# Kernel tuning notes

Hardware: AMD Instinct MI355X
Metric: run time of the kernel (lower is better)

## Reference

```python
import jax, jax.numpy as jnp
import numpy as np

N = 30000      # nodes
E = 480000     # edges
NF = 92        # node features
EF = 50        # edge features
D1 = 64        # dim1
D2 = 64        # dim2
L = 3          # conv_count
FC = 2         # fc_count
G = 256        # graphs in batch
EPS = 1e-5


def setup_inputs() -> dict:
    key = jax.random.key(0)
    ks = jax.random.split(key, 20)
    s = 0.05
    zd = 2 * D1 + EF  # CGConv concat dim
    inp = {
        "x": jax.random.normal(ks[0], (N, NF), jnp.float32),
        "edge_attr": jax.random.uniform(ks[1], (E, EF), jnp.float32),
        "lin0_w": jax.random.normal(ks[2], (NF, D1), jnp.float32) * s,
        "lin0_b": jnp.zeros((D1,), jnp.float32),
        "conv_wf": jax.random.normal(ks[3], (L, zd, D1), jnp.float32) * s,
        "conv_bf": jnp.zeros((L, D1), jnp.float32),
        "conv_ws": jax.random.normal(ks[4], (L, zd, D1), jnp.float32) * s,
        "conv_bs": jnp.zeros((L, D1), jnp.float32),
        "bn_gamma": jnp.ones((L, D1), jnp.float32),
        "bn_beta": jnp.zeros((L, D1), jnp.float32),
        "lin1_w": jax.random.normal(ks[5], (D1, D2), jnp.float32) * s,
        "lin1_b": jnp.zeros((D2,), jnp.float32),
        "fc_w": jax.random.normal(ks[6], (FC, D2, D2), jnp.float32) * s,
        "fc_b": jnp.zeros((FC, D2), jnp.float32),
        "lin2_w": jax.random.normal(ks[7], (D2, 1), jnp.float32) * s,
        "lin2_b": jnp.zeros((1,), jnp.float32),
        "edge_index": jax.random.randint(ks[8], (2, E), 0, N),
        "batch": jnp.sort(jax.random.randint(ks[9], (N,), 0, G)),
        "n_graphs": G,
    }
    return inp


def reference(x, edge_attr, lin0_w, lin0_b, conv_wf, conv_bf, conv_ws, conv_bs,
              bn_gamma, bn_beta, lin1_w, lin1_b, fc_w, fc_b, lin2_w, lin2_b,
              edge_index, batch, n_graphs):
    n = x.shape[0]
    src = edge_index[0]  # x_j (source)
    dst = edge_index[1]  # x_i (target, aggregation index)
    h = jax.nn.relu(x @ lin0_w + lin0_b)  # [N, D1]

    # per-target edge counts for mean aggregation (constant across layers)
    cnt = jax.ops.segment_sum(jnp.ones((src.shape[0],), h.dtype), dst, num_segments=n)
    cnt = jnp.maximum(cnt, 1.0)[:, None]

    for l in range(L):
        # z = [x_i || x_j || e_ij]  -> gated message sigmoid(Wf z) * softplus(Ws z)
        z = jnp.concatenate([h[dst], h[src], edge_attr], axis=-1)  # [E, 2*D1+EF]
        m = jax.nn.sigmoid(z @ conv_wf[l] + conv_bf[l]) * jax.nn.softplus(z @ conv_ws[l] + conv_bs[l])
        aggr = jax.ops.segment_sum(m, dst, num_segments=n) / cnt  # mean aggr [N, D1]
        # BatchNorm (training-mode batch stats, biased variance as in torch)
        mu = jnp.mean(aggr, axis=0)
        var = jnp.var(aggr, axis=0)
        aggr = (aggr - mu) * jax.lax.rsqrt(var + EPS) * bn_gamma[l] + bn_beta[l]
        h = jax.nn.relu(h + aggr)  # residual then outer ReLU

    # global mean pool over graphs
    gcnt = jnp.maximum(jax.ops.segment_sum(jnp.ones((n,), h.dtype), batch, num_segments=n_graphs), 1.0)[:, None]
    out = jax.ops.segment_sum(h, batch, num_segments=n_graphs) / gcnt  # [G, D1]

    out = jax.nn.relu(out @ lin1_w + lin1_b)
    for f in range(FC):
        out = jax.nn.relu(out @ fc_w[f] + fc_b[f])
    out = out @ lin2_w + lin2_b
    return out.reshape(-1)  # [G]
```

## Files before the change

### kernel.cpp

```cpp
#include <hip/hip_runtime.h>
#include <hip/hip_bf16.h>

#define N_NODES 30000
#define N_EDGES 480000
#define NFEAT 92
#define EFEAT 50
#define D1 64
#define ZD 178
#define NL 3
#define NG 256
#define BN_EPS 1e-5f
#define NTILES (N_EDGES / 16)
#define EDGE_BLOCKS 7500
#define EDGE_GRID 7504

#define LIN0_BLOCKS 512
#define CNT_BLOCKS 1875
#define WPREP_BLOCKS 96
#define SCAN_BLOCKS ((N_NODES + 255) / 256)

typedef __attribute__((ext_vector_type(8))) short bf16x8;
typedef __attribute__((ext_vector_type(8))) unsigned short u16x8;
typedef __attribute__((ext_vector_type(4))) unsigned short u16x4;
typedef __attribute__((ext_vector_type(4))) float f32x4;

static __device__ __forceinline__ unsigned short f2bf(float v) {
  __hip_bfloat16 b = __float2bfloat16(v);
  return *(unsigned short*)&b;
}
static __device__ __forceinline__ float bfu(unsigned short u) {
  union { unsigned int i; float f; } c;
  c.i = ((unsigned int)u) << 16;
  return c.f;
}

extern "C" __global__ void __launch_bounds__(256)
k_init(const float* __restrict__ x, const float* __restrict__ w,
       const float* __restrict__ b, float* __restrict__ h,
       const int* __restrict__ ei, int* __restrict__ cnt,
       const float* __restrict__ conv_wf, const float* __restrict__ conv_ws,
       unsigned short* __restrict__ Bp) {
  const int blk = blockIdx.x;
  if (blk < LIN0_BLOCKS) {
    const int lane = threadIdx.x & 63;
    const int wave = (blk * 256 + threadIdx.x) >> 6;
    const int nw = (LIN0_BLOCKS * 256) >> 6;
    float wreg[NFEAT];
#pragma unroll
    for (int k = 0; k < NFEAT; ++k) wreg[k] = w[k * D1 + lane];
    const float bj = b[lane];
    for (int i = wave; i < N_NODES; i += nw) {
      const float2* xr = (const float2*)(x + (size_t)i * NFEAT);
      float acc = bj;
#pragma unroll
      for (int k = 0; k < NFEAT / 2; ++k) {
        const float2 v = xr[k];
        acc = fmaf(v.x, wreg[2 * k], acc);
        acc = fmaf(v.y, wreg[2 * k + 1], acc);
      }
      h[(size_t)i * D1 + lane] = fmaxf(acc, 0.0f);
    }
  } else if (blk < LIN0_BLOCKS + CNT_BLOCKS) {
    const int e = (blk - LIN0_BLOCKS) * 256 + threadIdx.x;
    if (e < N_EDGES) atomicAdd(&cnt[ei[N_EDGES + e]], 1);
  } else {
    const int idx = (blk - LIN0_BLOCKS - CNT_BLOCKS) * 256 + threadIdx.x;
    const int j = idx & 7;
    const int lane = (idx >> 3) & 63;
    const int frag = (idx >> 9) & 15;
    const int l = idx >> 13;
    const int n = frag & 3;
    const int t = (frag >> 2) & 1;
    const int m = frag >> 3;
    const int k = t * 32 + (lane >> 4) * 8 + j;
    const int feat = (lane & 15) * 4 + n;
    float v = 0.0f;
    if (k < EFEAT) {
      const float* W = (m == 0) ? conv_wf : conv_ws;
      v = W[(size_t)l * ZD * D1 + (size_t)(128 + k) * D1 + feat];
    }
    Bp[idx] = f2bf(v);
  }
}

extern "C" __global__ void __launch_bounds__(256)
k_scan1(const int* __restrict__ cnt, int* __restrict__ lpre, int* __restrict__ ptot) {
  const int t = threadIdx.x;
  const int idx = blockIdx.x * 256 + t;
  const int v = (idx < N_NODES) ? cnt[idx] : 0;
  __shared__ int bs[256];
  bs[t] = v;
  __syncthreads();
  for (int off = 1; off < 256; off <<= 1) {
    int u = (t >= off) ? bs[t - off] : 0;
    __syncthreads();
    bs[t] += u;
    __syncthreads();
  }
  if (idx < N_NODES) lpre[idx] = bs[t] - v;
  if (t == 255) ptot[blockIdx.x] = bs[255];
}

extern "C" __global__ void __launch_bounds__(256)
k_scan23(const int* __restrict__ cnt, const int* __restrict__ lpre,
         const int* __restrict__ ptot, const int* __restrict__ batch,
         int* __restrict__ wptr, float* __restrict__ invc,
         int* __restrict__ grp) {
  __shared__ int bs[128];
  const int t = threadIdx.x;
  if (t < 128) bs[t] = (t < SCAN_BLOCKS) ? ptot[t] : 0;
  __syncthreads();
  for (int off = 1; off < 128; off <<= 1) {
    int u = 0;
    if (t < 128 && t >= off) u = bs[t - off];
    __syncthreads();
    if (t < 128 && t >= off) bs[t] += u;
    __syncthreads();
  }
  const int idx = blockIdx.x * 256 + t;
  if (idx >= N_NODES) return;
  const int bid = idx >> 8;
  const int boff = (bid == 0) ? 0 : bs[bid - 1];
  wptr[idx] = boff + lpre[idx];
  invc[idx] = 1.0f / fmaxf((float)cnt[idx], 1.0f);
  const int bt = batch[idx];
  if (idx == 0)
    for (int g = 0; g <= bt; ++g) grp[g] = 0;
  else {
    const int pb = batch[idx - 1];
    for (int g = pb + 1; g <= bt; ++g) grp[g] = idx;
  }
  if (idx == N_NODES - 1)
    for (int g = bt + 1; g <= NG; ++g) grp[g] = N_NODES;
}

extern "C" __global__ void __launch_bounds__(256)
k_build(const int* __restrict__ ei, int* __restrict__ wptr,
        int* __restrict__ srcs, int* __restrict__ dsts,
        const float* __restrict__ ea, unsigned short* __restrict__ eapb) {
  __shared__ int lpos[256];
  const int e0 = blockIdx.x * 256;
  {
    const int e = e0 + threadIdx.x;
    const int d = ei[N_EDGES + e];
    const int pos = atomicAdd(&wptr[d], 1);
    srcs[pos] = ei[e];
    dsts[pos] = d;
    lpos[threadIdx.x] = pos;
  }
  __syncthreads();
  const int l16 = threadIdx.x & 15;
  const int sub = threadIdx.x >> 4;
#pragma unroll
  for (int r = 0; r < 16; ++r) {
    const int eb = r * 16 + sub;
    const size_t ge = e0 + eb;
    const int pos = lpos[eb];
    unsigned short o0 = 0, o1 = 0, o2 = 0, o3 = 0;
    if (l16 < 12) {
      const float4 v = *(const float4*)(ea + ge * EFEAT + l16 * 4);
      o0 = f2bf(v.x); o1 = f2bf(v.y); o2 = f2bf(v.z); o3 = f2bf(v.w);
    } else if (l16 == 12) {
      const float2 v = *(const float2*)(ea + ge * EFEAT + 48);
      o0 = f2bf(v.x); o1 = f2bf(v.y);
    }
    u16x4 st;
    st[0] = o0; st[1] = o1; st[2] = o2; st[3] = o3;
    *(u16x4*)(eapb + ((size_t)pos << 6) + l16 * 4) = st;
  }
}

extern "C" __global__ void __launch_bounds__(256)
k_nodeproj(const float* __restrict__ hin, float* __restrict__ hout,
           const float* __restrict__ wfp, const float* __restrict__ wsm,
           unsigned short* __restrict__ projd_pk, unsigned short* __restrict__ projs_pk,
           const float* __restrict__ aggr, float* __restrict__ aggr_z,
           const float* __restrict__ invc,
           const float* __restrict__ musum, const float* __restrict__ sqsum,
           const float* __restrict__ gamma, const float* __restrict__ beta,
           int do_bn) {
  const int lane = threadIdx.x & 63;
  const int w = threadIdx.x >> 6;
  const float* W = (w < 2) ? wfp : wsm;
  const int roff = (w & 1) * 64;
  float wreg[D1];
#pragma unroll
  for (int k = 0; k < D1; ++k) wreg[k] = W[(size_t)(roff + k) * D1 + lane];
  unsigned short* pk = (w & 1) ? projs_pk : projd_pk;
  const int slot = (w < 2) ? 0 : 4;
  const int poff = (lane >> 2) * 8 + (lane & 3) + slot;
  float r = 0.0f, sh = 0.0f;
  if (do_bn) {
    const float mu = musum[lane] * (1.0f / N_NODES);
    const float var = sqsum[lane] * (1.0f / N_NODES) - mu * mu;
    r = gamma[lane] * rsqrtf(var + BN_EPS);
    sh = beta[lane] - mu * r;
  }
  __shared__ float hl[4][64];
  for (int i = blockIdx.x; i < N_NODES; i += gridDim.x) {
    float hv = hin[(size_t)i * D1 + lane];
    if (do_bn) {
      const float av = aggr[(size_t)i * D1 + lane] * invc[i];
      hv = fmaxf(hv + fmaf(av, r, sh), 0.0f);
      if (w == 0) hout[(size_t)i * D1 + lane] = hv;
    }
    if (w == 1) aggr_z[(size_t)i * D1 + lane] = 0.0f;
    hl[w][lane] = hv;
    __builtin_amdgcn_wave_barrier();
    const float4* hr = (const float4*)&hl[w][0];
    float acc = 0.0f;
#pragma unroll
    for (int k4 = 0; k4 < D1 / 4; ++k4) {
      const float4 v = hr[k4];
      acc = fmaf(v.x, wreg[4 * k4 + 0], acc);
      acc = fmaf(v.y, wreg[4 * k4 + 1], acc);
      acc = fmaf(v.z, wreg[4 * k4 + 2], acc);
      acc = fmaf(v.w, wreg[4 * k4 + 3], acc);
    }
    pk[(size_t)i * 128 + poff] = f2bf(acc);
    __builtin_amdgcn_wave_barrier();
  }
}

extern "C" __global__ void __launch_bounds__(256)
k_edgemm(const unsigned short* __restrict__ projd_pk,
         const unsigned short* __restrict__ projs_pk,
         const unsigned short* __restrict__ eapb,
         const int* __restrict__ srcs, const int* __restrict__ dsts,
         const unsigned short* __restrict__ Bp,
         const float* __restrict__ bfp, const float* __restrict__ bsp,
         float* __restrict__ aggr, float* __restrict__ musum,
         float* __restrict__ sqsum) {
  const int lane = threadIdx.x & 63;
  const int wv = threadIdx.x >> 6;
  const int col = lane & 15;
  const int quad = lane >> 4;
  __shared__ float mlds[4][16][68];

  const int vbid = (blockIdx.x & 7) * 938 + (blockIdx.x >> 3);
  if (blockIdx.x == 0 && wv == 0) {
    musum[lane] = 0.0f;
    sqsum[lane] = 0.0f;
  }
  if (vbid >= EDGE_BLOCKS) return;

  const int t = vbid * 4 + wv;
  const int base = t * 16;

  const int4 d4 = *(const int4*)(dsts + base + quad * 4);
  const int4 s4 = *(const int4*)(srcs + base + quad * 4);
  const int* dr = (const int*)&d4;
  const int* sr = (const int*)&s4;
  const bf16x8 Af0 = *(const bf16x8*)(eapb + ((size_t)(base + col) << 6) + quad * 8);
  const bf16x8 Af1 = *(const bf16x8*)(eapb + ((size_t)(base + col) << 6) + 32 + quad * 8);

  bf16x8 Bf[2][2][4];
#pragma unroll
  for (int m = 0; m < 2; ++m)
#pragma unroll
    for (int tt = 0; tt < 2; ++tt)
#pragma unroll
      for (int n = 0; n < 4; ++n)
        Bf[m][tt][n] = *(const bf16x8*)(Bp + ((((m * 2 + tt) * 4 + n) * 64 + lane) * 8));

  const f32x4 bf4 = *(const f32x4*)(bfp + col * 4);
  const f32x4 bs4 = *(const f32x4*)(bsp + col * 4);

  f32x4 aF[4], aS[4];
#pragma unroll
  for (int r = 0; r < 4; ++r) {
    const int d = dr[r];
    const int s = sr[r];
    const u16x8 pd = *(const u16x8*)(projd_pk + (size_t)d * 128 + col * 8);
    const u16x8 ss = *(const u16x8*)(projs_pk + (size_t)s * 128 + col * 8);
#pragma unroll
    for (int n = 0; n < 4; ++n) {
      aF[n][r] = bfu(pd[n]) + bfu(ss[n]) + bf4[n];
      aS[n][r] = bfu(pd[n + 4]) + bfu(ss[n + 4]) + bs4[n];
    }
  }

#pragma unroll
  for (int n = 0; n < 4; ++n) {
    aF[n] = __builtin_amdgcn_mfma_f32_16x16x32_bf16(Af0, Bf[0][0][n], aF[n], 0, 0, 0);
    aF[n] = __builtin_amdgcn_mfma_f32_16x16x32_bf16(Af1, Bf[0][1][n], aF[n], 0, 0, 0);
    aS[n] = __builtin_amdgcn_mfma_f32_16x16x32_bf16(Af0, Bf[1][0][n], aS[n], 0, 0, 0);
    aS[n] = __builtin_amdgcn_mfma_f32_16x16x32_bf16(Af1, Bf[1][1][n], aS[n], 0, 0, 0);
  }

#pragma unroll
  for (int r = 0; r < 4; ++r) {
    f32x4 mv;
#pragma unroll
    for (int n = 0; n < 4; ++n) {
      const float af = aF[n][r];
      const float as = aS[n][r];
      const float sg = __builtin_amdgcn_rcpf(1.0f + __expf(-af));
      const float sp = fmaxf(as, 0.0f) + __logf(1.0f + __expf(-fabsf(as)));
      mv[n] = sg * sp;
    }
    *(f32x4*)&mlds[wv][quad * 4 + r][col * 4] = mv;
  }
  __builtin_amdgcn_wave_barrier();

  float sum = 0.0f;
  int dcur = dsts[base];
#pragma unroll
  for (int p = 0; p < 16; ++p) {
    sum += mlds[wv][p][lane];
    const int dnxt = (p < 15) ? dsts[base + p + 1] : -1;
    if (dnxt != dcur) {
      atomicAdd(&aggr[(size_t)dcur * D1 + lane], sum);
      sum = 0.0f;
      dcur = dnxt;
    }
  }
}

extern "C" __global__ void __launch_bounds__(256)
k_stats(const float* __restrict__ aggr, const float* __restrict__ invc,
        float* __restrict__ musum, float* __restrict__ sqsum) {
  const int j = threadIdx.x & 63;
  const int rid = (blockIdx.x * blockDim.x + threadIdx.x) >> 6;
  const int rstr = (gridDim.x * blockDim.x) >> 6;
  float s = 0.0f, sq = 0.0f;
  for (int i = rid; i < N_NODES; i += rstr) {
    const float v = aggr[(size_t)i * D1 + j] * invc[i];
    s += v;
    sq = fmaf(v, v, sq);
  }
  __shared__ float ls[256], lq[256];
  ls[threadIdx.x] = s;
  lq[threadIdx.x] = sq;
  __syncthreads();
  if (threadIdx.x < 64) {
    s = ls[j] + ls[64 + j] + ls[128 + j] + ls[192 + j];
    sq = lq[j] + lq[64 + j] + lq[128 + j] + lq[192 + j];
    atomicAdd(&musum[j], s);
    atomicAdd(&sqsum[j], sq);
  }
}

extern "C" __global__ void __launch_bounds__(256)
k_poolmlp(const float* __restrict__ h, const float* __restrict__ aggr,
          const float* __restrict__ invc,
          const float* __restrict__ musum, const float* __restrict__ sqsum,
          const float* __restrict__ gamma, const float* __restrict__ beta,
          const int* __restrict__ grp,
          const float* __restrict__ lin1_w, const float* __restrict__ lin1_b,
          const float* __restrict__ fc_w, const float* __restrict__ fc_b,
          const float* __restrict__ lin2_w, const float* __restrict__ lin2_b,
          float* __restrict__ out) {
  const int g = blockIdx.x;
  const int lane = threadIdx.x & 63;
  const int wv = threadIdx.x >> 6;
  const float mu = musum[lane] * (1.0f / N_NODES);
  const float var = sqsum[lane] * (1.0f / N_NODES) - mu * mu;
  const float r = gamma[lane] * rsqrtf(var + BN_EPS);
  const float sh = beta[lane] - mu * r;
  const int s = grp[g], e = grp[g + 1];
  float acc = 0.0f;
  for (int i = s + wv; i < e; i += 4) {
    const float hv = h[(size_t)i * D1 + lane];
    const float av = aggr[(size_t)i * D1 + lane] * invc[i];
    acc += fmaxf(hv + fmaf(av, r, sh), 0.0f);
  }
  __shared__ float red[4][64];
  __shared__ float vin[64];
  red[wv][lane] = acc;
  __syncthreads();
  const int j = threadIdx.x;
  float v = 0.0f;
  if (j < 64) {
    const float inv = 1.0f / fmaxf((float)(e - s), 1.0f);
    v = (red[0][j] + red[1][j] + red[2][j] + red[3][j]) * inv;
  }
  for (int layer = 0; layer < 3; ++layer) {
    if (j < 64) vin[j] = v;
    __syncthreads();
    if (j < 64) {
      const float* W;
      const float* B;
      if (layer == 0) {
        W = lin1_w;
        B = lin1_b;
      } else {
        W = fc_w + (size_t)(layer - 1) * D1 * D1;
        B = fc_b + (size_t)(layer - 1) * D1;
      }
      float a2 = B[j];
#pragma unroll 16
      for (int k = 0; k < D1; ++k) a2 = fmaf(vin[k], W[k * D1 + j], a2);
      v = fmaxf(a2, 0.0f);
    }
    __syncthreads();
  }
  if (j < 64) {
    float p = v * lin2_w[j];
#pragma unroll
    for (int off = 32; off > 0; off >>= 1) p += __shfl_down(p, off);
    if (j == 0) out[g] = p + lin2_b[0];
  }
}

extern "C" void kernel_launch(void* const* d_in, const int* in_sizes, int n_in,
                              void* d_out, int out_size, void* d_ws, size_t ws_size,
                              hipStream_t stream) {
  const float* x        = (const float*)d_in[0];
  const float* ea       = (const float*)d_in[1];
  const float* lin0_w   = (const float*)d_in[2];
  const float* lin0_b   = (const float*)d_in[3];
  const float* conv_wf  = (const float*)d_in[4];
  const float* conv_bf  = (const float*)d_in[5];
  const float* conv_ws  = (const float*)d_in[6];
  const float* conv_bs  = (const float*)d_in[7];
  const float* bn_gamma = (const float*)d_in[8];
  const float* bn_beta  = (const float*)d_in[9];
  const float* lin1_w   = (const float*)d_in[10];
  const float* lin1_b   = (const float*)d_in[11];
  const float* fc_w     = (const float*)d_in[12];
  const float* fc_b     = (const float*)d_in[13];
  const float* lin2_w   = (const float*)d_in[14];
  const float* lin2_b   = (const float*)d_in[15];
  const int*   ei       = (const int*)d_in[16];
  const int*   batch    = (const int*)d_in[17];

  uintptr_t p = (uintptr_t)d_ws;
  auto alloc = [&](size_t bytes) {
    p = (p + 255) & ~(size_t)255;
    void* r = (void*)p;
    p += bytes;
    return r;
  };
  float* h0     = (float*)alloc((size_t)N_NODES * 64 * 4);
  float* h1     = (float*)alloc((size_t)N_NODES * 64 * 4);
  unsigned short* projd_pk = (unsigned short*)alloc((size_t)N_NODES * 128 * 2);
  unsigned short* projs_pk = (unsigned short*)alloc((size_t)N_NODES * 128 * 2);
  float* aggrA  = (float*)alloc((size_t)N_NODES * 64 * 4);
  float* aggrB  = (float*)alloc((size_t)N_NODES * 64 * 4);
  float* musum  = (float*)alloc(128 * 4);
  float* sqsum  = musum + 64;
  float* invc   = (float*)alloc((size_t)N_NODES * 4);
  int*   cnt    = (int*)alloc((size_t)N_NODES * 4);
  int*   lpre   = (int*)alloc((size_t)N_NODES * 4);
  int*   ptot   = (int*)alloc((size_t)SCAN_BLOCKS * 4);
  int*   wptr   = (int*)alloc((size_t)N_NODES * 4);
  int*   srcs   = (int*)alloc((size_t)N_EDGES * 4);
  int*   dsts   = (int*)alloc((size_t)N_EDGES * 4);
  int*   grp    = (int*)alloc((size_t)(NG + 1) * 4);
  unsigned short* eapb = (unsigned short*)alloc((size_t)N_EDGES * 64 * 2);
  unsigned short* Bp   = (unsigned short*)alloc((size_t)NL * 16 * 64 * 8 * 2);

  hipMemsetAsync(cnt, 0, N_NODES * sizeof(int), stream);
  k_init<<<LIN0_BLOCKS + CNT_BLOCKS + WPREP_BLOCKS, 256, 0, stream>>>(
      x, lin0_w, lin0_b, h0, ei, cnt, conv_wf, conv_ws, Bp);
  k_scan1<<<SCAN_BLOCKS, 256, 0, stream>>>(cnt, lpre, ptot);
  k_scan23<<<SCAN_BLOCKS, 256, 0, stream>>>(cnt, lpre, ptot, batch, wptr, invc, grp);
  k_build<<<N_EDGES / 256, 256, 0, stream>>>(ei, wptr, srcs, dsts, ea, eapb);

  float* aggr_of[NL] = {aggrA, aggrB, aggrA};
  const float* hin_of[NL]  = {h0, h0, h1};
  float* hout_of[NL]       = {h0, h1, h0};

  for (int l = 0; l < NL; ++l) {
    const float* wfl = conv_wf + (size_t)l * ZD * D1;
    const float* wsl = conv_ws + (size_t)l * ZD * D1;
    k_nodeproj<<<1024, 256, 0, stream>>>(
        hin_of[l], hout_of[l], wfl, wsl, projd_pk, projs_pk,
        (l == 0) ? nullptr : aggr_of[l - 1], aggr_of[l], invc, musum, sqsum,
        bn_gamma + (size_t)(l - 1) * D1, bn_beta + (size_t)(l - 1) * D1, l != 0);
    k_edgemm<<<EDGE_GRID, 256, 0, stream>>>(
        projd_pk, projs_pk, eapb, srcs, dsts,
        Bp + (size_t)l * 16 * 64 * 8,
        conv_bf + (size_t)l * D1, conv_bs + (size_t)l * D1,
        aggr_of[l], musum, sqsum);
    k_stats<<<256, 256, 0, stream>>>(aggr_of[l], invc, musum, sqsum);
  }

  k_poolmlp<<<NG, 256, 0, stream>>>(h0, aggr_of[2], invc, musum, sqsum,
                                    bn_gamma + (size_t)2 * D1, bn_beta + (size_t)2 * D1,
                                    grp, lin1_w, lin1_b, fc_w, fc_b,
                                    lin2_w, lin2_b, (float*)d_out);
}
```

Measured before the change: 624.1 us.

## Fuse layer-0 node projection into edge build kernel and pack dst/src pairs

The layer-0 node projection now runs as extra blocks inside the edge build (CSR scatter) kernel, which removes one launch and lets the two independent jobs overlap on the GPU. The separate src and dst index arrays are merged into one interleaved int2 array, so the edge kernel reads both with vector loads from one stream. The shared lpos buffer is reused as the projection scratch. The cost is a larger combined kernel, and the edge kernel now loads 8-byte pairs even when it only needs dst in the reduction loop.

```diff
diff --git a/kernel.cpp b/kernel.cpp
--- a/kernel.cpp
+++ b/kernel.cpp
@@ -18,6 +18,8 @@
 #define CNT_BLOCKS 1875
 #define WPREP_BLOCKS 96
 #define SCAN_BLOCKS ((N_NODES + 255) / 256)
+#define BUILD_BLOCKS 1875
+#define NP_BLOCKS 1024
 
 typedef __attribute__((ext_vector_type(8))) short bf16x8;
 typedef __attribute__((ext_vector_type(8))) unsigned short u16x8;
@@ -32,6 +34,56 @@
   union { unsigned int i; float f; } c;
   c.i = ((unsigned int)u) << 16;
   return c.f;
+}
+
+static __device__ __forceinline__ void nodeproj_body(
+    int blk0, int nblk, const float* __restrict__ hin, float* __restrict__ hout,
+    const float* __restrict__ wfp, const float* __restrict__ wsm,
+    unsigned short* __restrict__ projd_pk, unsigned short* __restrict__ projs_pk,
+    const float* __restrict__ aggr, float* __restrict__ aggr_z,
+    const float* __restrict__ invc, const float* __restrict__ musum,
+    const float* __restrict__ sqsum, const float* __restrict__ gamma,
+    const float* __restrict__ beta, int do_bn, float (*hl)[64]) {
+  const int lane = threadIdx.x & 63;
+  const int w = threadIdx.x >> 6;
+  const float* W = (w < 2) ? wfp : wsm;
+  const int roff = (w & 1) * 64;
+  float wreg[D1];
+#pragma unroll
+  for (int k = 0; k < D1; ++k) wreg[k] = W[(size_t)(roff + k) * D1 + lane];
+  unsigned short* pk = (w & 1) ? projs_pk : projd_pk;
+  const int slot = (w < 2) ? 0 : 4;
+  const int poff = (lane >> 2) * 8 + (lane & 3) + slot;
+  float r = 0.0f, sh = 0.0f;
+  if (do_bn) {
+    const float mu = musum[lane] * (1.0f / N_NODES);
+    const float var = sqsum[lane] * (1.0f / N_NODES) - mu * mu;
+    r = gamma[lane] * rsqrtf(var + BN_EPS);
+    sh = beta[lane] - mu * r;
+  }
+  for (int i = blk0; i < N_NODES; i += nblk) {
+    float hv = hin[(size_t)i * D1 + lane];
+    if (do_bn) {
+      const float av = aggr[(size_t)i * D1 + lane] * invc[i];
+      hv = fmaxf(hv + fmaf(av, r, sh), 0.0f);
+      if (w == 0) hout[(size_t)i * D1 + lane] = hv;
+    }
+    if (w == 1) aggr_z[(size_t)i * D1 + lane] = 0.0f;
+    hl[w][lane] = hv;
+    __builtin_amdgcn_wave_barrier();
+    const float4* hr = (const float4*)&hl[w][0];
+    float acc = 0.0f;
+#pragma unroll
+    for (int k4 = 0; k4 < D1 / 4; ++k4) {
+      const float4 v = hr[k4];
+      acc = fmaf(v.x, wreg[4 * k4 + 0], acc);
+      acc = fmaf(v.y, wreg[4 * k4 + 1], acc);
+      acc = fmaf(v.z, wreg[4 * k4 + 2], acc);
+      acc = fmaf(v.w, wreg[4 * k4 + 3], acc);
+    }
+    pk[(size_t)i * 128 + poff] = f2bf(acc);
+    __builtin_amdgcn_wave_barrier();
+  }
 }
 
 extern "C" __global__ void __launch_bounds__(256)
@@ -136,16 +188,24 @@
 
 extern "C" __global__ void __launch_bounds__(256)
 k_build(const int* __restrict__ ei, int* __restrict__ wptr,
-        int* __restrict__ srcs, int* __restrict__ dsts,
-        const float* __restrict__ ea, unsigned short* __restrict__ eapb) {
-  __shared__ int lpos[256];
+        int2* __restrict__ ds2, const float* __restrict__ ea,
+        unsigned short* __restrict__ eapb,
+        const float* __restrict__ h0, const float* __restrict__ wfl,
+        const float* __restrict__ wsl, unsigned short* __restrict__ projd_pk,
+        unsigned short* __restrict__ projs_pk, float* __restrict__ aggrA) {
+  __shared__ __align__(16) int lpos[256];
+  if (blockIdx.x >= BUILD_BLOCKS) {
+    nodeproj_body(blockIdx.x - BUILD_BLOCKS, NP_BLOCKS, h0, nullptr, wfl, wsl,
+                  projd_pk, projs_pk, nullptr, aggrA, nullptr, nullptr, nullptr,
+                  nullptr, nullptr, 0, (float(*)[64])lpos);
+    return;
+  }
   const int e0 = blockIdx.x * 256;
   {
     const int e = e0 + threadIdx.x;
     const int d = ei[N_EDGES + e];
     const int pos = atomicAdd(&wptr[d], 1);
-    srcs[pos] = ei[e];
-    dsts[pos] = d;
+    ds2[pos] = make_int2(d, ei[e]);
     lpos[threadIdx.x] = pos;
   }
   __syncthreads();
@@ -177,56 +237,17 @@
            const float* __restrict__ aggr, float* __restrict__ aggr_z,
            const float* __restrict__ invc,
            const float* __restrict__ musum, const float* __restrict__ sqsum,
-           const float* __restrict__ gamma, const float* __restrict__ beta,
-           int do_bn) {
-  const int lane = threadIdx.x & 63;
-  const int w = threadIdx.x >> 6;
-  const float* W = (w < 2) ? wfp : wsm;
-  const int roff = (w & 1) * 64;
-  float wreg[D1];
-#pragma unroll
-  for (int k = 0; k < D1; ++k) wreg[k] = W[(size_t)(roff + k) * D1 + lane];
-  unsigned short* pk = (w & 1) ? projs_pk : projd_pk;
-  const int slot = (w < 2) ? 0 : 4;
-  const int poff = (lane >> 2) * 8 + (lane & 3) + slot;
-  float r = 0.0f, sh = 0.0f;
-  if (do_bn) {
-    const float mu = musum[lane] * (1.0f / N_NODES);
-    const float var = sqsum[lane] * (1.0f / N_NODES) - mu * mu;
-    r = gamma[lane] * rsqrtf(var + BN_EPS);
-    sh = beta[lane] - mu * r;
-  }
+           const float* __restrict__ gamma, const float* __restrict__ beta) {
   __shared__ float hl[4][64];
-  for (int i = blockIdx.x; i < N_NODES; i += gridDim.x) {
-    float hv = hin[(size_t)i * D1 + lane];
-    if (do_bn) {
-      const float av = aggr[(size_t)i * D1 + lane] * invc[i];
-      hv = fmaxf(hv + fmaf(av, r, sh), 0.0f);
-      if (w == 0) hout[(size_t)i * D1 + lane] = hv;
-    }
-    if (w == 1) aggr_z[(size_t)i * D1 + lane] = 0.0f;
-    hl[w][lane] = hv;
-    __builtin_amdgcn_wave_barrier();
-    const float4* hr = (const float4*)&hl[w][0];
-    float acc = 0.0f;
-#pragma unroll
-    for (int k4 = 0; k4 < D1 / 4; ++k4) {
-      const float4 v = hr[k4];
-      acc = fmaf(v.x, wreg[4 * k4 + 0], acc);
-      acc = fmaf(v.y, wreg[4 * k4 + 1], acc);
-      acc = fmaf(v.z, wreg[4 * k4 + 2], acc);
-      acc = fmaf(v.w, wreg[4 * k4 + 3], acc);
-    }
-    pk[(size_t)i * 128 + poff] = f2bf(acc);
-    __builtin_amdgcn_wave_barrier();
-  }
+  nodeproj_body(blockIdx.x, gridDim.x, hin, hout, wfp, wsm, projd_pk, projs_pk,
+                aggr, aggr_z, invc, musum, sqsum, gamma, beta, 1, hl);
 }
 
 extern "C" __global__ void __launch_bounds__(256)
 k_edgemm(const unsigned short* __restrict__ projd_pk,
          const unsigned short* __restrict__ projs_pk,
          const unsigned short* __restrict__ eapb,
-         const int* __restrict__ srcs, const int* __restrict__ dsts,
+         const int2* __restrict__ ds2,
          const unsigned short* __restrict__ Bp,
          const float* __restrict__ bfp, const float* __restrict__ bsp,
          float* __restrict__ aggr, float* __restrict__ musum,
@@ -247,10 +268,10 @@
   const int t = vbid * 4 + wv;
   const int base = t * 16;
 
-  const int4 d4 = *(const int4*)(dsts + base + quad * 4);
-  const int4 s4 = *(const int4*)(srcs + base + quad * 4);
-  const int* dr = (const int*)&d4;
-  const int* sr = (const int*)&s4;
+  const int4 p01 = *(const int4*)(ds2 + base + quad * 4);
+  const int4 p23 = *(const int4*)(ds2 + base + quad * 4 + 2);
+  const int dr[4] = {p01.x, p01.z, p23.x, p23.z};
+  const int sr[4] = {p01.y, p01.w, p23.y, p23.w};
   const bf16x8 Af0 = *(const bf16x8*)(eapb + ((size_t)(base + col) << 6) + quad * 8);
   const bf16x8 Af1 = *(const bf16x8*)(eapb + ((size_t)(base + col) << 6) + 32 + quad * 8);
 
@@ -304,11 +325,11 @@
   __builtin_amdgcn_wave_barrier();
 
   float sum = 0.0f;
-  int dcur = dsts[base];
+  int dcur = ds2[base].x;
 #pragma unroll
   for (int p = 0; p < 16; ++p) {
     sum += mlds[wv][p][lane];
-    const int dnxt = (p < 15) ? dsts[base + p + 1] : -1;
+    const int dnxt = (p < 15) ? ds2[base + p + 1].x : -1;
     if (dnxt != dcur) {
       atomicAdd(&aggr[(size_t)dcur * D1 + lane], sum);
       sum = 0.0f;
@@ -445,8 +466,7 @@
   int*   lpre   = (int*)alloc((size_t)N_NODES * 4);
   int*   ptot   = (int*)alloc((size_t)SCAN_BLOCKS * 4);
   int*   wptr   = (int*)alloc((size_t)N_NODES * 4);
-  int*   srcs   = (int*)alloc((size_t)N_EDGES * 4);
-  int*   dsts   = (int*)alloc((size_t)N_EDGES * 4);
+  int2*  ds2    = (int2*)alloc((size_t)N_EDGES * 8);
   int*   grp    = (int*)alloc((size_t)(NG + 1) * 4);
   unsigned short* eapb = (unsigned short*)alloc((size_t)N_EDGES * 64 * 2);
   unsigned short* Bp   = (unsigned short*)alloc((size_t)NL * 16 * 64 * 8 * 2);
@@ -456,7 +476,8 @@
       x, lin0_w, lin0_b, h0, ei, cnt, conv_wf, conv_ws, Bp);
   k_scan1<<<SCAN_BLOCKS, 256, 0, stream>>>(cnt, lpre, ptot);
   k_scan23<<<SCAN_BLOCKS, 256, 0, stream>>>(cnt, lpre, ptot, batch, wptr, invc, grp);
-  k_build<<<N_EDGES / 256, 256, 0, stream>>>(ei, wptr, srcs, dsts, ea, eapb);
+  k_build<<<BUILD_BLOCKS + NP_BLOCKS, 256, 0, stream>>>(
+      ei, wptr, ds2, ea, eapb, h0, conv_wf, conv_ws, projd_pk, projs_pk, aggrA);
 
   float* aggr_of[NL] = {aggrA, aggrB, aggrA};
   const float* hin_of[NL]  = {h0, h0, h1};
@@ -465,12 +486,13 @@
   for (int l = 0; l < NL; ++l) {
     const float* wfl = conv_wf + (size_t)l * ZD * D1;
     const float* wsl = conv_ws + (size_t)l * ZD * D1;
-    k_nodeproj<<<1024, 256, 0, stream>>>(
-        hin_of[l], hout_of[l], wfl, wsl, projd_pk, projs_pk,
-        (l == 0) ? nullptr : aggr_of[l - 1], aggr_of[l], invc, musum, sqsum,
-        bn_gamma + (size_t)(l - 1) * D1, bn_beta + (size_t)(l - 1) * D1, l != 0);
+    if (l > 0)
+      k_nodeproj<<<1024, 256, 0, stream>>>(
+          hin_of[l], hout_of[l], wfl, wsl, projd_pk, projs_pk,
+          aggr_of[l - 1], aggr_of[l], invc, musum, sqsum,
+          bn_gamma + (size_t)(l - 1) * D1, bn_beta + (size_t)(l - 1) * D1);
     k_edgemm<<<EDGE_GRID, 256, 0, stream>>>(
-        projd_pk, projs_pk, eapb, srcs, dsts,
+        projd_pk, projs_pk, eapb, ds2,
         Bp + (size_t)l * 16 * 64 * 8,
         conv_bf + (size_t)l * D1, conv_bs + (size_t)l * D1,
         aggr_of[l], musum, sqsum);
```

Result: no change. 619.6 us (-0.7%).
